# Kernel tuning notes

Measured on AMD Instinct MI355X. Metric: run time of the kernel, lower is better.

The kernel has to match this reference:

```python
import jax, jax.numpy as jnp
import numpy as np

EPS = 1e-5      # BatchNorm2d default eps
SLOPE = 0.01    # F.leaky_relu default negative slope


def _bn(h, gamma, beta):
    # training-mode BatchNorm2d with batch=1: normalize per channel over the
    # N x N spatial extent (channels are the last axis here).
    mean = jnp.mean(h, axis=(0, 1))
    var = jnp.var(h, axis=(0, 1))  # biased variance, as torch uses for normalization
    return (h - mean) * jax.lax.rsqrt(var + EPS) * gamma + beta


def _block(h, W, b, gamma, beta):
    # 1x1 conv == per-position channel matmul; layout [N, N, C]
    h = jnp.einsum('nmc,oc->nmo', h, W) + b
    return jax.nn.leaky_relu(_bn(h, gamma, beta), SLOPE)


def setup_inputs() -> dict:
    key = jax.random.key(0)
    ks = jax.random.split(key, 12)
    N, C = 1536, 64
    H = [16, 16, 8, 8]  # nf * ratio
    x = jax.random.normal(ks[0], (N, C), dtype=jnp.float32)
    def w(k, o, i):
        return jax.random.normal(k, (o, i), dtype=jnp.float32) * (1.0 / np.sqrt(i))
    inp = {
        'x': x,
        'W1': w(ks[1], H[0], C),   'b1': jnp.zeros((H[0],), jnp.float32),
        'g1': jnp.ones((H[0],), jnp.float32), 'be1': jnp.zeros((H[0],), jnp.float32),
        'W2': w(ks[2], H[1], H[0]), 'b2': jnp.zeros((H[1],), jnp.float32),
        'g2': jnp.ones((H[1],), jnp.float32), 'be2': jnp.zeros((H[1],), jnp.float32),
        'W3': w(ks[3], H[2], H[1]), 'b3': jnp.zeros((H[2],), jnp.float32),
        'g3': jnp.ones((H[2],), jnp.float32), 'be3': jnp.zeros((H[2],), jnp.float32),
        'W4': w(ks[4], H[3], H[2]), 'b4': jnp.zeros((H[3],), jnp.float32),
        'g4': jnp.ones((H[3],), jnp.float32), 'be4': jnp.zeros((H[3],), jnp.float32),
        'W5': w(ks[5], 1, H[3]),    'b5': jnp.zeros((1,), jnp.float32),
    }
    return inp


def reference(x, W1, b1, g1, be1, W2, b2, g2, be2, W3, b3, g3, be3,
              W4, b4, g4, be4, W5, b5):
    # pairwise abs-diff adjacency features: [N, N, C]
    adj = jnp.abs(x[:, None, :] - x[None, :, :])
    h = _block(adj, W1, b1, g1, be1)
    h = _block(h, W2, b2, g2, be2)
    h = _block(h, W3, b3, g3, be3)
    h = _block(h, W4, b4, g4, be4)
    out = jnp.einsum('nmc,oc->nmo', h, W5) + b5  # [N, N, 1]
    return out[..., 0]  # [N, N]
```

## Files before the change

kernel.cpp:

```cpp
#include <hip/hip_runtime.h>
#include <stdint.h>


#define NPTS 1536
#define NTILES 4656
static constexpr float FNN   = 2359296.0f;
static constexpr float EPS   = 1e-5f;
static constexpr float SLOPE = 0.01f;
static constexpr float INV_M = 1.0f / 2359296.0f;

typedef __attribute__((ext_vector_type(8)))  short bf16x8;
typedef __attribute__((ext_vector_type(4)))  float f32x4;
typedef __attribute__((ext_vector_type(16))) float f32x16;
union frag8 { int4 i; bf16x8 v; };

__device__ __forceinline__ float bflo(unsigned u) {
    return __builtin_bit_cast(float, u << 16);
}
__device__ __forceinline__ float bfhi(unsigned u) {
    return __builtin_bit_cast(float, u & 0xffff0000u);
}
__device__ __forceinline__ unsigned short f2bf(float f) {
    unsigned u = __builtin_bit_cast(unsigned, f);
    u += 0x7fffu + ((u >> 16) & 1u);
    return (unsigned short)(u >> 16);
}
__device__ __forceinline__ unsigned pack2(float lo, float hi) {
    return (unsigned)f2bf(lo) | ((unsigned)f2bf(hi) << 16);
}
__device__ __forceinline__ unsigned packtr(float lo, float hi) {
    unsigned a = __builtin_bit_cast(unsigned, lo);
    unsigned b = __builtin_bit_cast(unsigned, hi);
#if __has_builtin(__builtin_amdgcn_perm)
    return __builtin_amdgcn_perm(b, a, 0x07060302u);
#else
    return (a >> 16) | (b & 0xffff0000u);
#endif
}
__device__ __forceinline__ float lrelu(float t) {
    return fmaxf(t, t * SLOPE);
}
__device__ __forceinline__ float4 ld4(const float* p) {
    return *(const float4*)p;
}
__device__ __forceinline__ unsigned shflx32(unsigned v) {
    return (unsigned)__shfl_xor((int)v, 32);
}

__device__ __forceinline__ int2 tri_decode(int t) {
    float disc = 37249.0f - 8.0f * (float)t;
    int mt = (int)((193.0f - sqrtf(disc)) * 0.5f);
    if (mt < 0) mt = 0;
    if (mt > 95) mt = 95;
    while (96 * (mt + 1) - ((mt + 1) * mt) / 2 <= t) mt++;
    while (96 * mt - (mt * (mt - 1)) / 2 > t) mt--;
    int nc = mt + (t - (96 * mt - (mt * (mt - 1)) / 2));
    return make_int2(mt, nc);
}

__device__ __forceinline__ void bn8_inline(
        const float* __restrict__ stats, const float* __restrict__ g,
        const float* __restrict__ be, float* sc, float* sh) {
#pragma unroll
    for (int c = 0; c < 8; c++) {
        float S = stats[c] + stats[16 + c] + stats[32 + c] + stats[48 + c];
        float Q = stats[8 + c] + stats[24 + c] + stats[40 + c] +
                  stats[56 + c];
        float mu  = S * INV_M;
        float var = fmaf(-mu, mu, Q * INV_M);
        float s   = g[c] * rsqrtf(var + EPS);
        sc[c] = s;
        sh[c] = fmaf(-mu, s, be[c]);
    }
}

__global__ __launch_bounds__(256) void k_prep(float* __restrict__ ws) {
    int t = blockIdx.x * 256 + threadIdx.x;
    if (t < 384) ws[t] = 0.0f;
}

__global__ __launch_bounds__(256) void k_layer1(
        const float* __restrict__ x, const float* __restrict__ W1,
        const float* __restrict__ b1, unsigned short* __restrict__ outb,
        float* __restrict__ stats) {
    int tid  = threadIdx.x;
    int lane = tid & 63;
    int wv   = tid >> 6;
    int gid  = blockIdx.x * 4 + wv;
    int2 tc  = tri_decode(gid);
    int mt   = tc.x;
    int nc   = tc.y;
    float wf = (mt == nc) ? 1.0f : 2.0f;
    int l15  = lane & 15;
    int quad = lane >> 4;
    int cb   = quad * 8;

    const float* wr = W1 + l15 * 64 + cb;
    float4 w0 = ld4(wr);
    float4 w1 = ld4(wr + 4);
    float4 w2 = ld4(wr + 32);
    float4 w3 = ld4(wr + 36);
    frag8 fb1, fb2;
    fb1.i = make_int4(pack2(w0.x, w0.y), pack2(w0.z, w0.w),
                      pack2(w1.x, w1.y), pack2(w1.z, w1.w));
    fb2.i = make_int4(pack2(w2.x, w2.y), pack2(w2.z, w2.w),
                      pack2(w3.x, w3.y), pack2(w3.z, w3.w));

    const float* xr = x + (mt * 16 + l15) * 64 + cb;
    float4 xa0 = ld4(xr);
    float4 xa1 = ld4(xr + 4);
    float4 xa2 = ld4(xr + 32);
    float4 xa3 = ld4(xr + 36);

    float4 b1v = ld4(b1 + quad * 4);
    float lsum[4] = {0.f, 0.f, 0.f, 0.f};
    float lssq[4] = {0.f, 0.f, 0.f, 0.f};

    int n0 = nc * 16;
    const float* xp = x + (size_t)n0 * 64 + cb;
    float4 uA0 = ld4(xp);
    float4 uA1 = ld4(xp + 4);
    float4 uA2 = ld4(xp + 32);
    float4 uA3 = ld4(xp + 36);
    const float* xq = x + (size_t)(n0 + 1) * 64 + cb;
    float4 uB0 = ld4(xq);
    float4 uB1 = ld4(xq + 4);
    float4 uB2 = ld4(xq + 32);
    float4 uB3 = ld4(xq + 36);

    auto body = [&](int i, float4& u0, float4& u1, float4& u2, float4& u3,
                    int pf) {
        frag8 fa1, fa2;
        fa1.i = make_int4(
            packtr(fabsf(xa0.x - u0.x), fabsf(xa0.y - u0.y)),
            packtr(fabsf(xa0.z - u0.z), fabsf(xa0.w - u0.w)),
            packtr(fabsf(xa1.x - u1.x), fabsf(xa1.y - u1.y)),
            packtr(fabsf(xa1.z - u1.z), fabsf(xa1.w - u1.w)));
        fa2.i = make_int4(
            packtr(fabsf(xa2.x - u2.x), fabsf(xa2.y - u2.y)),
            packtr(fabsf(xa2.z - u2.z), fabsf(xa2.w - u2.w)),
            packtr(fabsf(xa3.x - u3.x), fabsf(xa3.y - u3.y)),
            packtr(fabsf(xa3.z - u3.z), fabsf(xa3.w - u3.w)));
        const float* xf = x + (size_t)pf * 64 + cb;
        u0 = ld4(xf);
        u1 = ld4(xf + 4);
        u2 = ld4(xf + 32);
        u3 = ld4(xf + 36);
        f32x4 acc = {b1v.x, b1v.y, b1v.z, b1v.w};
        acc = __builtin_amdgcn_mfma_f32_16x16x32_bf16(fb1.v, fa1.v, acc, 0, 0, 0);
        acc = __builtin_amdgcn_mfma_f32_16x16x32_bf16(fb2.v, fa2.v, acc, 0, 0, 0);
        size_t pos = (size_t)gid * 256 + (size_t)i * 16 + l15;
#pragma unroll
        for (int r = 0; r < 4; r++) {
            lsum[r] += acc[r];
            lssq[r] = fmaf(acc[r], acc[r], lssq[r]);
        }
        *(uint2*)(outb + pos * 16 + quad * 4) =
            make_uint2(pack2(acc[0], acc[1]), pack2(acc[2], acc[3]));
    };

#pragma unroll 1
    for (int i = 0; i < 16; i += 2) {
        int pfA = n0 + ((i + 2 < 16) ? i + 2 : 15);
        int pfB = n0 + ((i + 3 < 16) ? i + 3 : 15);
        body(i,     uA0, uA1, uA2, uA3, pfA);
        body(i + 1, uB0, uB1, uB2, uB3, pfB);
    }

#pragma unroll
    for (int off = 1; off < 16; off <<= 1) {
#pragma unroll
        for (int r = 0; r < 4; r++) {
            lsum[r] += __shfl_xor(lsum[r], off);
            lssq[r] += __shfl_xor(lssq[r], off);
        }
    }
    __shared__ float red[4][32];
    if (l15 == 0) {
#pragma unroll
        for (int r = 0; r < 4; r++) {
            red[wv][quad * 4 + r]      = lsum[r] * wf;
            red[wv][16 + quad * 4 + r] = lssq[r] * wf;
        }
    }
    __syncthreads();
    if (tid < 32) {
        float v = red[0][tid] + red[1][tid] + red[2][tid] + red[3][tid];
        atomicAdd(stats + (blockIdx.x & 3) * 32 + tid, v);
    }
}

__global__ __launch_bounds__(256) void k_stats2(
        const unsigned short* __restrict__ h1,
        const float* __restrict__ stats1, const float* __restrict__ g1,
        const float* __restrict__ be1, const float* __restrict__ W2,
        float* __restrict__ raw2) {
    int tid  = threadIdx.x;
    int lane = tid & 63;
    int wv   = tid >> 6;
    int pc   = lane & 31;
    int kh   = lane >> 5;
    int gid  = blockIdx.x * 4 + wv;
    int2 tc  = tri_decode(gid);
    float wf = (tc.x == tc.y) ? 1.0f : 2.0f;

    float sc[8], sh[8];
#pragma unroll
    for (int j = 0; j < 8; j++) {
        int c = kh * 8 + j;
        float S = stats1[c] + stats1[32 + c] + stats1[64 + c] + stats1[96 + c];
        float Q = stats1[16 + c] + stats1[48 + c] + stats1[80 + c] +
                  stats1[112 + c];
        float mu  = S * INV_M;
        float var = fmaf(-mu, mu, Q * INV_M);
        float s   = g1[c] * rsqrtf(var + EPS);
        sc[j] = s;
        sh[j] = fmaf(-mu, s, be1[c]);
    }
    frag8 fw2; fw2.i = make_int4(0, 0, 0, 0);
    if (pc < 16) {
        const float* w = W2 + pc * 16 + kh * 8;
        float4 wa = ld4(w), wb = ld4(w + 4);
        fw2.i = make_int4(pack2(wa.x, wa.y), pack2(wa.z, wa.w),
                          pack2(wb.x, wb.y), pack2(wb.z, wb.w));
    }
    f32x16 z;
#pragma unroll
    for (int r = 0; r < 16; r++) z[r] = 0.0f;

    float sum[8], ssq[8];
#pragma unroll
    for (int r = 0; r < 8; r++) { sum[r] = 0.f; ssq[r] = 0.f; }

    size_t tile0 = (size_t)gid * 8;
    const unsigned short* ptr = h1 + (tile0 * 32 + pc) * 16 + kh * 8;

    auto proc = [&](uint4 v) {
        float a0 = bflo(v.x), a1 = bfhi(v.x);
        float a2 = bflo(v.y), a3 = bfhi(v.y);
        float a4 = bflo(v.z), a5 = bfhi(v.z);
        float a6 = bflo(v.w), a7 = bfhi(v.w);
        a0 = lrelu(fmaf(a0, sc[0], sh[0]));
        a1 = lrelu(fmaf(a1, sc[1], sh[1]));
        a2 = lrelu(fmaf(a2, sc[2], sh[2]));
        a3 = lrelu(fmaf(a3, sc[3], sh[3]));
        a4 = lrelu(fmaf(a4, sc[4], sh[4]));
        a5 = lrelu(fmaf(a5, sc[5], sh[5]));
        a6 = lrelu(fmaf(a6, sc[6], sh[6]));
        a7 = lrelu(fmaf(a7, sc[7], sh[7]));
        frag8 fb;
        fb.i = make_int4(packtr(a0, a1), packtr(a2, a3),
                         packtr(a4, a5), packtr(a6, a7));
        f32x16 d = __builtin_amdgcn_mfma_f32_32x32x16_bf16(fw2.v, fb.v, z, 0, 0, 0);
#pragma unroll
        for (int r = 0; r < 8; r++) {
            sum[r] += d[r];
            ssq[r] = fmaf(d[r], d[r], ssq[r]);
        }
    };

    uint4 vA = *(const uint4*)(ptr);
    uint4 vB = *(const uint4*)(ptr + 512);
#pragma unroll 1
    for (int p = 0; p < 4; p++) {
        uint4 nA = vA, nB = vB;
        if (p < 3) {
            nA = *(const uint4*)(ptr + (size_t)(2 * p + 2) * 512);
            nB = *(const uint4*)(ptr + (size_t)(2 * p + 3) * 512);
        }
        proc(vA);
        proc(vB);
        vA = nA; vB = nB;
    }

#pragma unroll
    for (int off = 1; off < 32; off <<= 1) {
#pragma unroll
        for (int r = 0; r < 8; r++) {
            sum[r] += __shfl_xor(sum[r], off);
            ssq[r] += __shfl_xor(ssq[r], off);
        }
    }
    __shared__ float red[4][32];
    if (pc == 0) {
#pragma unroll
        for (int r = 0; r < 8; r++) {
            int o = (r & 3) + 8 * (r >> 2) + 4 * kh;
            red[wv][o]      = sum[r] * wf;
            red[wv][16 + o] = ssq[r] * wf;
        }
    }
    __syncthreads();
    if (tid < 32) {
        float v = red[0][tid] + red[1][tid] + red[2][tid] + red[3][tid];
        atomicAdd(raw2 + (blockIdx.x & 3) * 32 + tid, v);
    }
}

__global__ __launch_bounds__(256) void k_fuse3(
        const unsigned short* __restrict__ h1,
        unsigned short* __restrict__ h3out,
        const float* __restrict__ stats1, const float* __restrict__ g1,
        const float* __restrict__ be1, const float* __restrict__ W2,
        const float* __restrict__ raw2, const float* __restrict__ g2,
        const float* __restrict__ be2, const float* __restrict__ b2,
        const float* __restrict__ W3, const float* __restrict__ b3,
        float* __restrict__ stats3) {
    int tid  = threadIdx.x;
    int lane = tid & 63;
    int wv   = tid >> 6;
    int pc   = lane & 31;
    int kh   = lane >> 5;
    int gid  = blockIdx.x * 4 + wv;
    int2 tc  = tri_decode(gid);
    float wf = (tc.x == tc.y) ? 1.0f : 2.0f;

    float sc[8], sh[8];
#pragma unroll
    for (int j = 0; j < 8; j++) {
        int c = kh * 8 + j;
        float S = stats1[c] + stats1[32 + c] + stats1[64 + c] + stats1[96 + c];
        float Q = stats1[16 + c] + stats1[48 + c] + stats1[80 + c] +
                  stats1[112 + c];
        float mu  = S * INV_M;
        float var = fmaf(-mu, mu, Q * INV_M);
        float s   = g1[c] * rsqrtf(var + EPS);
        sc[j] = s;
        sh[j] = fmaf(-mu, s, be1[c]);
    }
    float sc2[8], sh2[8];
#pragma unroll
    for (int r = 0; r < 8; r++) {
        int c = (r & 3) + 8 * (r >> 2) + 4 * kh;
        float S = raw2[c] + raw2[32 + c] + raw2[64 + c] + raw2[96 + c];
        float Q = raw2[16 + c] + raw2[48 + c] + raw2[80 + c] + raw2[112 + c];
        float bc = b2[c];
        float sm = S + FNN * bc;
        float sq = Q + 2.0f * bc * S + FNN * bc * bc;
        float mu  = sm * INV_M;
        float var = fmaf(-mu, mu, sq * INV_M);
        float s   = g2[c] * rsqrtf(var + EPS);
        float shv = fmaf(-mu, s, be2[c]);
        sc2[r] = s;
        sh2[r] = fmaf(s, bc, shv);
    }
    frag8 fw2; fw2.i = make_int4(0, 0, 0, 0);
    if (pc < 16) {
        const float* w = W2 + pc * 16 + kh * 8;
        float4 wa = ld4(w), wb = ld4(w + 4);
        fw2.i = make_int4(pack2(wa.x, wa.y), pack2(wa.z, wa.w),
                          pack2(wb.x, wb.y), pack2(wb.z, wb.w));
    }
    frag8 fw3; fw3.i = make_int4(0, 0, 0, 0);
    if (pc < 8) {
        const float* w = W3 + pc * 16 + kh * 8;
        float4 wa = ld4(w), wb = ld4(w + 4);
        fw3.i = make_int4(pack2(wa.x, wa.y), pack2(wa.z, wa.w),
                          pack2(wb.x, wb.y), pack2(wb.z, wb.w));
    }
    float b3r[4];
#pragma unroll
    for (int r = 0; r < 4; r++) b3r[r] = b3[kh * 4 + r];

    f32x16 z;
#pragma unroll
    for (int r = 0; r < 16; r++) z[r] = 0.0f;

    float sum3[4] = {0.f, 0.f, 0.f, 0.f}, ssq3[4] = {0.f, 0.f, 0.f, 0.f};

    size_t tile0 = (size_t)gid * 8;
    const unsigned short* ptr = h1 + (tile0 * 32 + pc) * 16 + kh * 8;

    uint4 v0 = *(const uint4*)(ptr);
    uint4 v1 = *(const uint4*)(ptr + 512);
#pragma unroll 1
    for (int it = 0; it < 8; it++) {
        uint4 nx = v0;
        if (it + 2 < 8)
            nx = *(const uint4*)(ptr + (size_t)(it + 2) * 512);
        float a0 = bflo(v0.x), a1 = bfhi(v0.x);
        float a2 = bflo(v0.y), a3 = bfhi(v0.y);
        float a4 = bflo(v0.z), a5 = bfhi(v0.z);
        float a6 = bflo(v0.w), a7 = bfhi(v0.w);
        a0 = lrelu(fmaf(a0, sc[0], sh[0]));
        a1 = lrelu(fmaf(a1, sc[1], sh[1]));
        a2 = lrelu(fmaf(a2, sc[2], sh[2]));
        a3 = lrelu(fmaf(a3, sc[3], sh[3]));
        a4 = lrelu(fmaf(a4, sc[4], sh[4]));
        a5 = lrelu(fmaf(a5, sc[5], sh[5]));
        a6 = lrelu(fmaf(a6, sc[6], sh[6]));
        a7 = lrelu(fmaf(a7, sc[7], sh[7]));
        frag8 fb;
        fb.i = make_int4(packtr(a0, a1), packtr(a2, a3),
                         packtr(a4, a5), packtr(a6, a7));
        f32x16 d = __builtin_amdgcn_mfma_f32_32x32x16_bf16(fw2.v, fb.v, z, 0, 0, 0);
        float t0 = lrelu(fmaf(d[0], sc2[0], sh2[0]));
        float t1 = lrelu(fmaf(d[1], sc2[1], sh2[1]));
        float t2 = lrelu(fmaf(d[2], sc2[2], sh2[2]));
        float t3 = lrelu(fmaf(d[3], sc2[3], sh2[3]));
        float t4 = lrelu(fmaf(d[4], sc2[4], sh2[4]));
        float t5 = lrelu(fmaf(d[5], sc2[5], sh2[5]));
        float t6 = lrelu(fmaf(d[6], sc2[6], sh2[6]));
        float t7 = lrelu(fmaf(d[7], sc2[7], sh2[7]));
        unsigned w0 = packtr(t0, t1), w1 = packtr(t2, t3);
        unsigned w2 = packtr(t4, t5), w3 = packtr(t6, t7);
        unsigned p0 = kh ? w0 : w2;
        unsigned p1 = kh ? w1 : w3;
        unsigned q0 = shflx32(p0);
        unsigned q1 = shflx32(p1);
        frag8 fb2;
        fb2.i = make_int4(kh ? q0 : w0, kh ? q1 : w1,
                          kh ? w2 : q0, kh ? w3 : q1);
        f32x16 d2 = __builtin_amdgcn_mfma_f32_32x32x16_bf16(fw3.v, fb2.v, z, 0, 0, 0);
        float h0 = d2[0] + b3r[0];
        float h1v = d2[1] + b3r[1];
        float h2 = d2[2] + b3r[2];
        float h3v = d2[3] + b3r[3];
        sum3[0] += h0;  ssq3[0] = fmaf(h0, h0, ssq3[0]);
        sum3[1] += h1v; ssq3[1] = fmaf(h1v, h1v, ssq3[1]);
        sum3[2] += h2;  ssq3[2] = fmaf(h2, h2, ssq3[2]);
        sum3[3] += h3v; ssq3[3] = fmaf(h3v, h3v, ssq3[3]);
        size_t pos = (tile0 + it) * 32 + pc;
        *(uint2*)(h3out + pos * 8 + kh * 4) =
            make_uint2(pack2(h0, h1v), pack2(h2, h3v));
        v0 = v1; v1 = nx;
    }
#pragma unroll
    for (int off = 1; off < 32; off <<= 1) {
#pragma unroll
        for (int r = 0; r < 4; r++) {
            sum3[r] += __shfl_xor(sum3[r], off);
            ssq3[r] += __shfl_xor(ssq3[r], off);
        }
    }
    __shared__ float red[4][16];
    if (pc == 0) {
#pragma unroll
        for (int r = 0; r < 4; r++) {
            red[wv][kh * 4 + r]     = sum3[r] * wf;
            red[wv][8 + kh * 4 + r] = ssq3[r] * wf;
        }
    }
    __syncthreads();
    if (tid < 16) {
        float v = red[0][tid] + red[1][tid] + red[2][tid] + red[3][tid];
        atomicAdd(stats3 + (blockIdx.x & 3) * 16 + tid, v);
    }
}

__global__ __launch_bounds__(256) void k_stats4(
        const unsigned short* __restrict__ h3,
        const float* __restrict__ stats3, const float* __restrict__ g3,
        const float* __restrict__ be3, const float* __restrict__ W4,
        const float* __restrict__ b4, float* __restrict__ stats4) {
    int tid = threadIdx.x;
    int og1 = tid & 1;

    float wtile[4];
#pragma unroll
    for (int p = 0; p < 4; p++) {
        int2 tc = tri_decode(blockIdx.x * 4 + p);
        wtile[p] = (tc.x == tc.y) ? 1.0f : 2.0f;
    }

    float sc[8], sh[8];
    bn8_inline(stats3, g3, be3, sc, sh);

    float w[4][8];
#pragma unroll
    for (int j = 0; j < 4; j++) {
        const float* wr = W4 + (og1 * 4 + j) * 8;
        float4 v0 = ld4(wr);
        float4 v1 = ld4(wr + 4);
        w[j][0] = v0.x; w[j][1] = v0.y; w[j][2] = v0.z; w[j][3] = v0.w;
        w[j][4] = v1.x; w[j][5] = v1.y; w[j][6] = v1.z; w[j][7] = v1.w;
    }
    float bi[4];
#pragma unroll
    for (int j = 0; j < 4; j++) bi[j] = b4[og1 * 4 + j];

    float sum[4] = {0.f, 0.f, 0.f, 0.f}, ssq[4] = {0.f, 0.f, 0.f, 0.f};

    size_t p0 = (size_t)blockIdx.x * 1024 + (tid >> 1);
    const uint4* src = (const uint4*)h3 + p0;

    auto proc = [&](uint4 v, float wf) {
        float a[8];
        a[0] = bflo(v.x); a[1] = bfhi(v.x); a[2] = bflo(v.y); a[3] = bfhi(v.y);
        a[4] = bflo(v.z); a[5] = bfhi(v.z); a[6] = bflo(v.w); a[7] = bfhi(v.w);
#pragma unroll
        for (int c = 0; c < 8; c++)
            a[c] = lrelu(fmaf(a[c], sc[c], sh[c]));
        float d[4] = {bi[0], bi[1], bi[2], bi[3]};
#pragma unroll
        for (int c = 0; c < 8; c++) {
#pragma unroll
            for (int j = 0; j < 4; j++)
                d[j] = fmaf(a[c], w[j][c], d[j]);
        }
#pragma unroll
        for (int j = 0; j < 4; j++) {
            float wd = wf * d[j];
            sum[j] += wd;
            ssq[j] = fmaf(wd, d[j], ssq[j]);
        }
    };

    uint4 vA = src[0];
    uint4 vB = src[128];
#pragma unroll 1
    for (int p = 0; p < 4; p++) {
        uint4 nA = vA, nB = vB;
        if (p < 3) {
            nA = src[(size_t)(2 * p + 2) * 128];
            nB = src[(size_t)(2 * p + 3) * 128];
        }
        proc(vA, wtile[p]);
        proc(vB, wtile[p]);
        vA = nA; vB = nB;
    }
#pragma unroll
    for (int off = 2; off < 64; off <<= 1) {
#pragma unroll
        for (int j = 0; j < 4; j++) {
            sum[j] += __shfl_xor(sum[j], off);
            ssq[j] += __shfl_xor(ssq[j], off);
        }
    }
    __shared__ float red[4][16];
    int wv = tid >> 6, lane = tid & 63;
    if (lane < 2) {
#pragma unroll
        for (int j = 0; j < 4; j++) {
            red[wv][og1 * 4 + j]     = sum[j];
            red[wv][8 + og1 * 4 + j] = ssq[j];
        }
    }
    __syncthreads();
    if (tid < 16) {
        float v = red[0][tid] + red[1][tid] + red[2][tid] + red[3][tid];
        atomicAdd(stats4 + (blockIdx.x & 3) * 16 + tid, v);
    }
}

__global__ __launch_bounds__(256) void k_last(
        const unsigned short* __restrict__ h3,
        const float* __restrict__ stats3, const float* __restrict__ g3,
        const float* __restrict__ be3, const float* __restrict__ stats4,
        const float* __restrict__ g4, const float* __restrict__ be4,
        const float* __restrict__ W4, const float* __restrict__ b4,
        const float* __restrict__ W5, const float* __restrict__ b5,
        float* __restrict__ out) {
    int tid = threadIdx.x;

    size_t p0 = (size_t)blockIdx.x * 1024 + tid;
    const uint4* src = (const uint4*)h3 + p0;
    uint4 vv[4];
    vv[0] = src[0];
    vv[1] = src[256];
    vv[2] = src[512];
    vv[3] = src[768];

    float sc3[8], sh3[8];
    bn8_inline(stats3, g3, be3, sc3, sh3);

    float w4f[8][8], b4f[8], w5[8];
#pragma unroll
    for (int o = 0; o < 8; o++) {
        float S = stats4[o] + stats4[16 + o] + stats4[32 + o] + stats4[48 + o];
        float Q = stats4[8 + o] + stats4[24 + o] + stats4[40 + o] +
                  stats4[56 + o];
        float mu  = S * INV_M;
        float var = fmaf(-mu, mu, Q * INV_M);
        float s   = g4[o] * rsqrtf(var + EPS);
        float shv = fmaf(-mu, s, be4[o]);
        b4f[o] = fmaf(s, b4[o], shv);
        const float* wr = W4 + o * 8;
        float4 v0 = ld4(wr);
        float4 v1 = ld4(wr + 4);
        w4f[o][0] = s * v0.x; w4f[o][1] = s * v0.y;
        w4f[o][2] = s * v0.z; w4f[o][3] = s * v0.w;
        w4f[o][4] = s * v1.x; w4f[o][5] = s * v1.y;
        w4f[o][6] = s * v1.z; w4f[o][7] = s * v1.w;
        w5[o] = W5[o];
    }
    float b5v = b5[0];

    int nl = tid >> 4, ml = tid & 15;
    int2 tcs[4];
#pragma unroll
    for (int it = 0; it < 4; it++)
        tcs[it] = tri_decode(blockIdx.x * 4 + it);

    __shared__ float T[4][272];

#pragma unroll
    for (int it = 0; it < 4; it++) {
        uint4 va = vv[it];
        float a[8];
        a[0] = bflo(va.x); a[1] = bfhi(va.x); a[2] = bflo(va.y); a[3] = bfhi(va.y);
        a[4] = bflo(va.z); a[5] = bfhi(va.z); a[6] = bflo(va.w); a[7] = bfhi(va.w);
#pragma unroll
        for (int c = 0; c < 8; c++)
            a[c] = lrelu(fmaf(a[c], sc3[c], sh3[c]));
        float acc = b5v;
#pragma unroll
        for (int o = 0; o < 8; o++) {
            float h = b4f[o];
#pragma unroll
            for (int c = 0; c < 8; c++)
                h = fmaf(a[c], w4f[o][c], h);
            acc = fmaf(lrelu(h), w5[o], acc);
        }
        int gn = tcs[it].y * 16 + nl;
        int gm = tcs[it].x * 16 + ml;
        out[(size_t)gn * NPTS + gm] = acc;
        T[it][nl * 17 + ml] = acc;
    }
    __syncthreads();
#pragma unroll
    for (int it = 0; it < 4; it++) {
        float mv = T[it][ml * 17 + nl];
        out[(size_t)(tcs[it].x * 16 + nl) * NPTS + tcs[it].y * 16 + ml] = mv;
    }
}

extern "C" void kernel_launch(void* const* d_in, const int* in_sizes, int n_in,
                              void* d_out, int out_size, void* d_ws,
                              size_t ws_size, hipStream_t stream) {
    const float* x   = (const float*)d_in[0];
    const float* W1  = (const float*)d_in[1];
    const float* b1  = (const float*)d_in[2];
    const float* g1  = (const float*)d_in[3];
    const float* be1 = (const float*)d_in[4];
    const float* W2  = (const float*)d_in[5];
    const float* b2  = (const float*)d_in[6];
    const float* g2  = (const float*)d_in[7];
    const float* be2 = (const float*)d_in[8];
    const float* W3  = (const float*)d_in[9];
    const float* b3  = (const float*)d_in[10];
    const float* g3  = (const float*)d_in[11];
    const float* be3 = (const float*)d_in[12];
    const float* W4  = (const float*)d_in[13];
    const float* b4  = (const float*)d_in[14];
    const float* g4  = (const float*)d_in[15];
    const float* be4 = (const float*)d_in[16];
    const float* W5  = (const float*)d_in[17];
    const float* b5  = (const float*)d_in[18];

    float* ws     = (float*)d_ws;
    float* stats1 = ws + 0;
    float* raw2   = ws + 128;
    float* stats3 = ws + 256;
    float* stats4 = ws + 320;
    unsigned short* bufA = (unsigned short*)((char*)d_ws + 8192);
    unsigned short* bufB =
        (unsigned short*)((char*)d_ws + 8192 + (size_t)NTILES * 256 * 32);

    k_prep<<<2, 256, 0, stream>>>(ws);
    k_layer1<<<1164, 256, 0, stream>>>(x, W1, b1, bufA, stats1);
    k_stats2<<<1164, 256, 0, stream>>>(bufA, stats1, g1, be1, W2, raw2);
    k_fuse3<<<1164, 256, 0, stream>>>(bufA, bufB, stats1, g1, be1, W2,
                                      raw2, g2, be2, b2, W3, b3, stats3);
    k_stats4<<<1164, 256, 0, stream>>>(bufB, stats3, g3, be3, W4, b4, stats4);
    k_last<<<1164, 256, 0, stream>>>(bufB, stats3, g3, be3, stats4, g4, be4,
                                     W4, b4, W5, b5, (float*)d_out);
}
```

Before: 188.2 us.

## Fuse all layers into one cooperative kernel keeping activations in LDS

Replaces the five-kernel pipeline with a single cooperative kernel of 256 blocks. Each block owns up to 19 triangle tiles and keeps their layer-1 activations in shared memory, using grid-wide syncs between the BatchNorm statistics passes. This removes the global-memory round trips for the intermediate bf16 buffers and several kernel launches. The cost is very large LDS use (about 152KB per block), one block per CU with only 8 waves, and serialized grid barriers that may hurt latency hiding.

```diff
diff --git a/kernel.cpp b/kernel.cpp
--- a/kernel.cpp
+++ b/kernel.cpp
@@ -1,9 +1,14 @@
 #include <hip/hip_runtime.h>
+#include <hip/hip_cooperative_groups.h>
 #include <stdint.h>
+
+namespace cg = cooperative_groups;
 
 
 #define NPTS 1536
 #define NTILES 4656
+#define NBLK 256
+#define NTMAX 19
 static constexpr float FNN   = 2359296.0f;
 static constexpr float EPS   = 1e-5f;
 static constexpr float SLOPE = 0.01f;
@@ -79,549 +84,497 @@
     if (t < 384) ws[t] = 0.0f;
 }
 
-__global__ __launch_bounds__(256) void k_layer1(
-        const float* __restrict__ x, const float* __restrict__ W1,
-        const float* __restrict__ b1, unsigned short* __restrict__ outb,
-        float* __restrict__ stats) {
+__global__ __launch_bounds__(512, 2) void k_mega(
+        const float* __restrict__ x,
+        const float* __restrict__ W1, const float* __restrict__ b1,
+        const float* __restrict__ g1, const float* __restrict__ be1,
+        const float* __restrict__ W2, const float* __restrict__ b2,
+        const float* __restrict__ g2, const float* __restrict__ be2,
+        const float* __restrict__ W3, const float* __restrict__ b3,
+        const float* __restrict__ g3, const float* __restrict__ be3,
+        const float* __restrict__ W4, const float* __restrict__ b4,
+        const float* __restrict__ g4, const float* __restrict__ be4,
+        const float* __restrict__ W5, const float* __restrict__ b5,
+        float* __restrict__ out, float* __restrict__ ws) {
+
+    __shared__ unsigned short hbuf[NTMAX * 4096];
+    __shared__ float red[8][32];
+    __shared__ float Tm[2][272];
+    __shared__ int tdesc[NTMAX];
+
+    cg::grid_group grid = cg::this_grid();
+
     int tid  = threadIdx.x;
+    int bid  = blockIdx.x;
+    int w    = tid >> 6;
     int lane = tid & 63;
-    int wv   = tid >> 6;
-    int gid  = blockIdx.x * 4 + wv;
-    int2 tc  = tri_decode(gid);
-    int mt   = tc.x;
-    int nc   = tc.y;
-    float wf = (mt == nc) ? 1.0f : 2.0f;
-    int l15  = lane & 15;
-    int quad = lane >> 4;
-    int cb   = quad * 8;
-
-    const float* wr = W1 + l15 * 64 + cb;
-    float4 w0 = ld4(wr);
-    float4 w1 = ld4(wr + 4);
-    float4 w2 = ld4(wr + 32);
-    float4 w3 = ld4(wr + 36);
-    frag8 fb1, fb2;
-    fb1.i = make_int4(pack2(w0.x, w0.y), pack2(w0.z, w0.w),
-                      pack2(w1.x, w1.y), pack2(w1.z, w1.w));
-    fb2.i = make_int4(pack2(w2.x, w2.y), pack2(w2.z, w2.w),
-                      pack2(w3.x, w3.y), pack2(w3.z, w3.w));
-
-    const float* xr = x + (mt * 16 + l15) * 64 + cb;
-    float4 xa0 = ld4(xr);
-    float4 xa1 = ld4(xr + 4);
-    float4 xa2 = ld4(xr + 32);
-    float4 xa3 = ld4(xr + 36);
-
-    float4 b1v = ld4(b1 + quad * 4);
-    float lsum[4] = {0.f, 0.f, 0.f, 0.f};
-    float lssq[4] = {0.f, 0.f, 0.f, 0.f};
-
-    int n0 = nc * 16;
-    const float* xp = x + (size_t)n0 * 64 + cb;
-    float4 uA0 = ld4(xp);
-    float4 uA1 = ld4(xp + 4);
-    float4 uA2 = ld4(xp + 32);
-    float4 uA3 = ld4(xp + 36);
-    const float* xq = x + (size_t)(n0 + 1) * 64 + cb;
-    float4 uB0 = ld4(xq);
-    float4 uB1 = ld4(xq + 4);
-    float4 uB2 = ld4(xq + 32);
-    float4 uB3 = ld4(xq + 36);
-
-    auto body = [&](int i, float4& u0, float4& u1, float4& u2, float4& u3,
-                    int pf) {
-        frag8 fa1, fa2;
-        fa1.i = make_int4(
-            packtr(fabsf(xa0.x - u0.x), fabsf(xa0.y - u0.y)),
-            packtr(fabsf(xa0.z - u0.z), fabsf(xa0.w - u0.w)),
-            packtr(fabsf(xa1.x - u1.x), fabsf(xa1.y - u1.y)),
-            packtr(fabsf(xa1.z - u1.z), fabsf(xa1.w - u1.w)));
-        fa2.i = make_int4(
-            packtr(fabsf(xa2.x - u2.x), fabsf(xa2.y - u2.y)),
-            packtr(fabsf(xa2.z - u2.z), fabsf(xa2.w - u2.w)),
-            packtr(fabsf(xa3.x - u3.x), fabsf(xa3.y - u3.y)),
-            packtr(fabsf(xa3.z - u3.z), fabsf(xa3.w - u3.w)));
-        const float* xf = x + (size_t)pf * 64 + cb;
-        u0 = ld4(xf);
-        u1 = ld4(xf + 4);
-        u2 = ld4(xf + 32);
-        u3 = ld4(xf + 36);
-        f32x4 acc = {b1v.x, b1v.y, b1v.z, b1v.w};
-        acc = __builtin_amdgcn_mfma_f32_16x16x32_bf16(fb1.v, fa1.v, acc, 0, 0, 0);
-        acc = __builtin_amdgcn_mfma_f32_16x16x32_bf16(fb2.v, fa2.v, acc, 0, 0, 0);
-        size_t pos = (size_t)gid * 256 + (size_t)i * 16 + l15;
-#pragma unroll
-        for (int r = 0; r < 4; r++) {
-            lsum[r] += acc[r];
-            lssq[r] = fmaf(acc[r], acc[r], lssq[r]);
-        }
-        *(uint2*)(outb + pos * 16 + quad * 4) =
-            make_uint2(pack2(acc[0], acc[1]), pack2(acc[2], acc[3]));
-    };
-
-#pragma unroll 1
-    for (int i = 0; i < 16; i += 2) {
-        int pfA = n0 + ((i + 2 < 16) ? i + 2 : 15);
-        int pfB = n0 + ((i + 3 < 16) ? i + 3 : 15);
-        body(i,     uA0, uA1, uA2, uA3, pfA);
-        body(i + 1, uB0, uB1, uB2, uB3, pfB);
-    }
-
-#pragma unroll
-    for (int off = 1; off < 16; off <<= 1) {
-#pragma unroll
-        for (int r = 0; r < 4; r++) {
-            lsum[r] += __shfl_xor(lsum[r], off);
-            lssq[r] += __shfl_xor(lssq[r], off);
-        }
-    }
-    __shared__ float red[4][32];
-    if (l15 == 0) {
-#pragma unroll
-        for (int r = 0; r < 4; r++) {
-            red[wv][quad * 4 + r]      = lsum[r] * wf;
-            red[wv][16 + quad * 4 + r] = lssq[r] * wf;
-        }
+    int NT   = 18 + (bid < 48 ? 1 : 0);
+
+    float* stats1 = ws;
+    float* raw2   = ws + 128;
+    float* stats3 = ws + 256;
+    float* stats4 = ws + 320;
+    int rep32 = (bid & 3) * 32;
+    int rep16 = (bid & 3) * 16;
+
+    if (tid < NT) {
+        int2 tc = tri_decode(bid + NBLK * tid);
+        tdesc[tid] = (tc.x << 8) | tc.y;
     }
     __syncthreads();
-    if (tid < 32) {
-        float v = red[0][tid] + red[1][tid] + red[2][tid] + red[3][tid];
-        atomicAdd(stats + (blockIdx.x & 3) * 32 + tid, v);
+
+    {
+        int l15 = lane & 15, quad = lane >> 4, cb = quad * 8;
+        const float* wr = W1 + l15 * 64 + cb;
+        float4 w0 = ld4(wr);
+        float4 w1v = ld4(wr + 4);
+        float4 w2v = ld4(wr + 32);
+        float4 w3v = ld4(wr + 36);
+        frag8 fb1, fb2;
+        fb1.i = make_int4(pack2(w0.x, w0.y), pack2(w0.z, w0.w),
+                          pack2(w1v.x, w1v.y), pack2(w1v.z, w1v.w));
+        fb2.i = make_int4(pack2(w2v.x, w2v.y), pack2(w2v.z, w2v.w),
+                          pack2(w3v.x, w3v.y), pack2(w3v.z, w3v.w));
+        float4 b1v = ld4(b1 + quad * 4);
+        float lsum[4] = {0.f, 0.f, 0.f, 0.f};
+        float lssq[4] = {0.f, 0.f, 0.f, 0.f};
+
+#pragma unroll 1
+        for (int i = 0; i < NT; i++) {
+            int td = tdesc[i];
+            int mt = td >> 8, nc = td & 255;
+            float wf = (mt == nc) ? 1.0f : 2.0f;
+            const float* xr = x + (mt * 16 + l15) * 64 + cb;
+            float4 xa0 = ld4(xr);
+            float4 xa1 = ld4(xr + 4);
+            float4 xa2 = ld4(xr + 32);
+            float4 xa3 = ld4(xr + 36);
+            int n0 = nc * 16;
+#pragma unroll
+            for (int jj = 0; jj < 2; jj++) {
+                int j = 2 * w + jj;
+                const float* xp = x + (size_t)(n0 + j) * 64 + cb;
+                float4 u0 = ld4(xp);
+                float4 u1 = ld4(xp + 4);
+                float4 u2 = ld4(xp + 32);
+                float4 u3 = ld4(xp + 36);
+                frag8 fa1, fa2;
+                fa1.i = make_int4(
+                    packtr(fabsf(xa0.x - u0.x), fabsf(xa0.y - u0.y)),
+                    packtr(fabsf(xa0.z - u0.z), fabsf(xa0.w - u0.w)),
+                    packtr(fabsf(xa1.x - u1.x), fabsf(xa1.y - u1.y)),
+                    packtr(fabsf(xa1.z - u1.z), fabsf(xa1.w - u1.w)));
+                fa2.i = make_int4(
+                    packtr(fabsf(xa2.x - u2.x), fabsf(xa2.y - u2.y)),
+                    packtr(fabsf(xa2.z - u2.z), fabsf(xa2.w - u2.w)),
+                    packtr(fabsf(xa3.x - u3.x), fabsf(xa3.y - u3.y)),
+                    packtr(fabsf(xa3.z - u3.z), fabsf(xa3.w - u3.w)));
+                f32x4 acc = {b1v.x, b1v.y, b1v.z, b1v.w};
+                acc = __builtin_amdgcn_mfma_f32_16x16x32_bf16(fb1.v, fa1.v,
+                                                              acc, 0, 0, 0);
+                acc = __builtin_amdgcn_mfma_f32_16x16x32_bf16(fb2.v, fa2.v,
+                                                              acc, 0, 0, 0);
+#pragma unroll
+                for (int r = 0; r < 4; r++) {
+                    float wa = wf * acc[r];
+                    lsum[r] += wa;
+                    lssq[r] = fmaf(wa, acc[r], lssq[r]);
+                }
+                *(uint2*)(hbuf + i * 4096 + j * 256 + l15 * 16 + quad * 4) =
+                    make_uint2(pack2(acc[0], acc[1]), pack2(acc[2], acc[3]));
+            }
+        }
+#pragma unroll
+        for (int off = 1; off < 16; off <<= 1) {
+#pragma unroll
+            for (int r = 0; r < 4; r++) {
+                lsum[r] += __shfl_xor(lsum[r], off);
+                lssq[r] += __shfl_xor(lssq[r], off);
+            }
+        }
+        if (l15 == 0) {
+#pragma unroll
+            for (int r = 0; r < 4; r++) {
+                red[w][quad * 4 + r]      = lsum[r];
+                red[w][16 + quad * 4 + r] = lssq[r];
+            }
+        }
+        __syncthreads();
+        if (tid < 32) {
+            float v = 0.f;
+#pragma unroll
+            for (int k = 0; k < 8; k++) v += red[k][tid];
+            atomicAdd(stats1 + rep32 + tid, v);
+        }
     }
-}
-
-__global__ __launch_bounds__(256) void k_stats2(
-        const unsigned short* __restrict__ h1,
-        const float* __restrict__ stats1, const float* __restrict__ g1,
-        const float* __restrict__ be1, const float* __restrict__ W2,
-        float* __restrict__ raw2) {
-    int tid  = threadIdx.x;
-    int lane = tid & 63;
-    int wv   = tid >> 6;
-    int pc   = lane & 31;
-    int kh   = lane >> 5;
-    int gid  = blockIdx.x * 4 + wv;
-    int2 tc  = tri_decode(gid);
-    float wf = (tc.x == tc.y) ? 1.0f : 2.0f;
-
-    float sc[8], sh[8];
-#pragma unroll
-    for (int j = 0; j < 8; j++) {
-        int c = kh * 8 + j;
-        float S = stats1[c] + stats1[32 + c] + stats1[64 + c] + stats1[96 + c];
-        float Q = stats1[16 + c] + stats1[48 + c] + stats1[80 + c] +
-                  stats1[112 + c];
-        float mu  = S * INV_M;
-        float var = fmaf(-mu, mu, Q * INV_M);
-        float s   = g1[c] * rsqrtf(var + EPS);
-        sc[j] = s;
-        sh[j] = fmaf(-mu, s, be1[c]);
+    grid.sync();
+
+    {
+        int pc = lane & 31, kh = lane >> 5;
+        float sc[8], sh[8];
+#pragma unroll
+        for (int jc = 0; jc < 8; jc++) {
+            int c = kh * 8 + jc;
+            float S = stats1[c] + stats1[32 + c] + stats1[64 + c] +
+                      stats1[96 + c];
+            float Q = stats1[16 + c] + stats1[48 + c] + stats1[80 + c] +
+                      stats1[112 + c];
+            float mu  = S * INV_M;
+            float var = fmaf(-mu, mu, Q * INV_M);
+            float s   = g1[c] * rsqrtf(var + EPS);
+            sc[jc] = s;
+            sh[jc] = fmaf(-mu, s, be1[c]);
+        }
+        frag8 fw2; fw2.i = make_int4(0, 0, 0, 0);
+        if (pc < 16) {
+            const float* wp = W2 + pc * 16 + kh * 8;
+            float4 wa = ld4(wp), wb = ld4(wp + 4);
+            fw2.i = make_int4(pack2(wa.x, wa.y), pack2(wa.z, wa.w),
+                              pack2(wb.x, wb.y), pack2(wb.z, wb.w));
+        }
+        f32x16 z;
+#pragma unroll
+        for (int r = 0; r < 16; r++) z[r] = 0.0f;
+        float sum2[8], ssq2[8];
+#pragma unroll
+        for (int r = 0; r < 8; r++) { sum2[r] = 0.f; ssq2[r] = 0.f; }
+
+#pragma unroll 1
+        for (int i = 0; i < NT; i++) {
+            int td = tdesc[i];
+            float wf = ((td >> 8) == (td & 255)) ? 1.0f : 2.0f;
+            uint4 v = *(const uint4*)(hbuf + i * 4096 + w * 512 + pc * 16 +
+                                      kh * 8);
+            float a0 = bflo(v.x), a1 = bfhi(v.x);
+            float a2 = bflo(v.y), a3 = bfhi(v.y);
+            float a4 = bflo(v.z), a5 = bfhi(v.z);
+            float a6 = bflo(v.w), a7 = bfhi(v.w);
+            a0 = lrelu(fmaf(a0, sc[0], sh[0]));
+            a1 = lrelu(fmaf(a1, sc[1], sh[1]));
+            a2 = lrelu(fmaf(a2, sc[2], sh[2]));
+            a3 = lrelu(fmaf(a3, sc[3], sh[3]));
+            a4 = lrelu(fmaf(a4, sc[4], sh[4]));
+            a5 = lrelu(fmaf(a5, sc[5], sh[5]));
+            a6 = lrelu(fmaf(a6, sc[6], sh[6]));
+            a7 = lrelu(fmaf(a7, sc[7], sh[7]));
+            frag8 fbv;
+            fbv.i = make_int4(packtr(a0, a1), packtr(a2, a3),
+                              packtr(a4, a5), packtr(a6, a7));
+            f32x16 d = __builtin_amdgcn_mfma_f32_32x32x16_bf16(fw2.v, fbv.v,
+                                                               z, 0, 0, 0);
+#pragma unroll
+            for (int r = 0; r < 8; r++) {
+                float dv = d[r];
+                float wd = wf * dv;
+                sum2[r] += wd;
+                ssq2[r] = fmaf(wd, dv, ssq2[r]);
+            }
+        }
+#pragma unroll
+        for (int off = 1; off < 32; off <<= 1) {
+#pragma unroll
+            for (int r = 0; r < 8; r++) {
+                sum2[r] += __shfl_xor(sum2[r], off);
+                ssq2[r] += __shfl_xor(ssq2[r], off);
+            }
+        }
+        if (pc == 0) {
+#pragma unroll
+            for (int r = 0; r < 8; r++) {
+                int o = (r & 3) + 8 * (r >> 2) + 4 * kh;
+                red[w][o]      = sum2[r];
+                red[w][16 + o] = ssq2[r];
+            }
+        }
+        __syncthreads();
+        if (tid < 32) {
+            float v = 0.f;
+#pragma unroll
+            for (int k = 0; k < 8; k++) v += red[k][tid];
+            atomicAdd(raw2 + rep32 + tid, v);
+        }
     }
-    frag8 fw2; fw2.i = make_int4(0, 0, 0, 0);
-    if (pc < 16) {
-        const float* w = W2 + pc * 16 + kh * 8;
-        float4 wa = ld4(w), wb = ld4(w + 4);
-        fw2.i = make_int4(pack2(wa.x, wa.y), pack2(wa.z, wa.w),
-                          pack2(wb.x, wb.y), pack2(wb.z, wb.w));
+    grid.sync();
+
+    {
+        int pc = lane & 31, kh = lane >> 5;
+        float sc[8], sh[8];
+#pragma unroll
+        for (int jc = 0; jc < 8; jc++) {
+            int c = kh * 8 + jc;
+            float S = stats1[c] + stats1[32 + c] + stats1[64 + c] +
+                      stats1[96 + c];
+            float Q = stats1[16 + c] + stats1[48 + c] + stats1[80 + c] +
+                      stats1[112 + c];
+            float mu  = S * INV_M;
+            float var = fmaf(-mu, mu, Q * INV_M);
+            float s   = g1[c] * rsqrtf(var + EPS);
+            sc[jc] = s;
+            sh[jc] = fmaf(-mu, s, be1[c]);
+        }
+        float sc2[8], sh2[8];
+#pragma unroll
+        for (int r = 0; r < 8; r++) {
+            int c = (r & 3) + 8 * (r >> 2) + 4 * kh;
+            float S = raw2[c] + raw2[32 + c] + raw2[64 + c] + raw2[96 + c];
+            float Q = raw2[16 + c] + raw2[48 + c] + raw2[80 + c] +
+                      raw2[112 + c];
+            float bc = b2[c];
+            float sm = S + FNN * bc;
+            float sq = Q + 2.0f * bc * S + FNN * bc * bc;
+            float mu  = sm * INV_M;
+            float var = fmaf(-mu, mu, sq * INV_M);
+            float s   = g2[c] * rsqrtf(var + EPS);
+            float shv = fmaf(-mu, s, be2[c]);
+            sc2[r] = s;
+            sh2[r] = fmaf(s, bc, shv);
+        }
+        frag8 fw2; fw2.i = make_int4(0, 0, 0, 0);
+        if (pc < 16) {
+            const float* wp = W2 + pc * 16 + kh * 8;
+            float4 wa = ld4(wp), wb = ld4(wp + 4);
+            fw2.i = make_int4(pack2(wa.x, wa.y), pack2(wa.z, wa.w),
+                              pack2(wb.x, wb.y), pack2(wb.z, wb.w));
+        }
+        frag8 fw3; fw3.i = make_int4(0, 0, 0, 0);
+        if (pc < 8) {
+            const float* wp = W3 + pc * 16 + kh * 8;
+            float4 wa = ld4(wp), wb = ld4(wp + 4);
+            fw3.i = make_int4(pack2(wa.x, wa.y), pack2(wa.z, wa.w),
+                              pack2(wb.x, wb.y), pack2(wb.z, wb.w));
+        }
+        float b3r[4];
+#pragma unroll
+        for (int r = 0; r < 4; r++) b3r[r] = b3[kh * 4 + r];
+        f32x16 z;
+#pragma unroll
+        for (int r = 0; r < 16; r++) z[r] = 0.0f;
+        float sum3[4] = {0.f, 0.f, 0.f, 0.f};
+        float ssq3[4] = {0.f, 0.f, 0.f, 0.f};
+
+#pragma unroll 1
+        for (int i = 0; i < NT; i++) {
+            int td = tdesc[i];
+            float wf = ((td >> 8) == (td & 255)) ? 1.0f : 2.0f;
+            uint4 v = *(const uint4*)(hbuf + i * 4096 + w * 512 + pc * 16 +
+                                      kh * 8);
+            __syncthreads();
+            float a0 = bflo(v.x), a1 = bfhi(v.x);
+            float a2 = bflo(v.y), a3 = bfhi(v.y);
+            float a4 = bflo(v.z), a5 = bfhi(v.z);
+            float a6 = bflo(v.w), a7 = bfhi(v.w);
+            a0 = lrelu(fmaf(a0, sc[0], sh[0]));
+            a1 = lrelu(fmaf(a1, sc[1], sh[1]));
+            a2 = lrelu(fmaf(a2, sc[2], sh[2]));
+            a3 = lrelu(fmaf(a3, sc[3], sh[3]));
+            a4 = lrelu(fmaf(a4, sc[4], sh[4]));
+            a5 = lrelu(fmaf(a5, sc[5], sh[5]));
+            a6 = lrelu(fmaf(a6, sc[6], sh[6]));
+            a7 = lrelu(fmaf(a7, sc[7], sh[7]));
+            frag8 fbv;
+            fbv.i = make_int4(packtr(a0, a1), packtr(a2, a3),
+                              packtr(a4, a5), packtr(a6, a7));
+            f32x16 d = __builtin_amdgcn_mfma_f32_32x32x16_bf16(fw2.v, fbv.v,
+                                                               z, 0, 0, 0);
+            float t0 = lrelu(fmaf(d[0], sc2[0], sh2[0]));
+            float t1 = lrelu(fmaf(d[1], sc2[1], sh2[1]));
+            float t2 = lrelu(fmaf(d[2], sc2[2], sh2[2]));
+            float t3 = lrelu(fmaf(d[3], sc2[3], sh2[3]));
+            float t4 = lrelu(fmaf(d[4], sc2[4], sh2[4]));
+            float t5 = lrelu(fmaf(d[5], sc2[5], sh2[5]));
+            float t6 = lrelu(fmaf(d[6], sc2[6], sh2[6]));
+            float t7 = lrelu(fmaf(d[7], sc2[7], sh2[7]));
+            unsigned e0 = packtr(t0, t1), e1 = packtr(t2, t3);
+            unsigned e2 = packtr(t4, t5), e3 = packtr(t6, t7);
+            unsigned p0 = kh ? e0 : e2;
+            unsigned p1 = kh ? e1 : e3;
+            unsigned q0 = shflx32(p0);
+            unsigned q1 = shflx32(p1);
+            frag8 fb2;
+            fb2.i = make_int4(kh ? q0 : e0, kh ? q1 : e1,
+                              kh ? e2 : q0, kh ? e3 : q1);
+            f32x16 d2 = __builtin_amdgcn_mfma_f32_32x32x16_bf16(fw3.v, fb2.v,
+                                                                z, 0, 0, 0);
+            float h0  = d2[0] + b3r[0];
+            float h1v = d2[1] + b3r[1];
+            float h2v = d2[2] + b3r[2];
+            float h3v = d2[3] + b3r[3];
+            float wh;
+            wh = wf * h0;  sum3[0] += wh; ssq3[0] = fmaf(wh, h0,  ssq3[0]);
+            wh = wf * h1v; sum3[1] += wh; ssq3[1] = fmaf(wh, h1v, ssq3[1]);
+            wh = wf * h2v; sum3[2] += wh; ssq3[2] = fmaf(wh, h2v, ssq3[2]);
+            wh = wf * h3v; sum3[3] += wh; ssq3[3] = fmaf(wh, h3v, ssq3[3]);
+            *(uint2*)(hbuf + i * 4096 + 2048 + w * 256 + pc * 8 + kh * 4) =
+                make_uint2(pack2(h0, h1v), pack2(h2v, h3v));
+        }
+#pragma unroll
+        for (int off = 1; off < 32; off <<= 1) {
+#pragma unroll
+            for (int r = 0; r < 4; r++) {
+                sum3[r] += __shfl_xor(sum3[r], off);
+                ssq3[r] += __shfl_xor(ssq3[r], off);
+            }
+        }
+        if (pc == 0) {
+#pragma unroll
+            for (int r = 0; r < 4; r++) {
+                red[w][kh * 4 + r]     = sum3[r];
+                red[w][8 + kh * 4 + r] = ssq3[r];
+            }
+        }
+        __syncthreads();
+        if (tid < 16) {
+            float v = 0.f;
+#pragma unroll
+            for (int k = 0; k < 8; k++) v += red[k][tid];
+            atomicAdd(stats3 + rep16 + tid, v);
+        }
     }
-    f32x16 z;
-#pragma unroll
-    for (int r = 0; r < 16; r++) z[r] = 0.0f;
-
-    float sum[8], ssq[8];
-#pragma unroll
-    for (int r = 0; r < 8; r++) { sum[r] = 0.f; ssq[r] = 0.f; }
-
-    size_t tile0 = (size_t)gid * 8;
-    const unsigned short* ptr = h1 + (tile0 * 32 + pc) * 16 + kh * 8;
-
-    auto proc = [&](uint4 v) {
-        float a0 = bflo(v.x), a1 = bfhi(v.x);
-        float a2 = bflo(v.y), a3 = bfhi(v.y);
-        float a4 = bflo(v.z), a5 = bfhi(v.z);
-        float a6 = bflo(v.w), a7 = bfhi(v.w);
-        a0 = lrelu(fmaf(a0, sc[0], sh[0]));
-        a1 = lrelu(fmaf(a1, sc[1], sh[1]));
-        a2 = lrelu(fmaf(a2, sc[2], sh[2]));
-        a3 = lrelu(fmaf(a3, sc[3], sh[3]));
-        a4 = lrelu(fmaf(a4, sc[4], sh[4]));
-        a5 = lrelu(fmaf(a5, sc[5], sh[5]));
-        a6 = lrelu(fmaf(a6, sc[6], sh[6]));
-        a7 = lrelu(fmaf(a7, sc[7], sh[7]));
-        frag8 fb;
-        fb.i = make_int4(packtr(a0, a1), packtr(a2, a3),
-                         packtr(a4, a5), packtr(a6, a7));
-        f32x16 d = __builtin_amdgcn_mfma_f32_32x32x16_bf16(fw2.v, fb.v, z, 0, 0, 0);
-#pragma unroll
-        for (int r = 0; r < 8; r++) {
-            sum[r] += d[r];
-            ssq[r] = fmaf(d[r], d[r], ssq[r]);
-        }
-    };
-
-    uint4 vA = *(const uint4*)(ptr);
-    uint4 vB = *(const uint4*)(ptr + 512);
+    grid.sync();
+
+    {
+        float sc3[8], sh3[8];
+        bn8_inline(stats3, g3, be3, sc3, sh3);
+        int og = tid >> 8;
+        int p  = tid & 255;
+        float wv4[4][8], bi[4];
+#pragma unroll
+        for (int jv = 0; jv < 4; jv++) {
+            const float* wr = W4 + (og * 4 + jv) * 8;
+            float4 v0 = ld4(wr);
+            float4 v1 = ld4(wr + 4);
+            wv4[jv][0] = v0.x; wv4[jv][1] = v0.y;
+            wv4[jv][2] = v0.z; wv4[jv][3] = v0.w;
+            wv4[jv][4] = v1.x; wv4[jv][5] = v1.y;
+            wv4[jv][6] = v1.z; wv4[jv][7] = v1.w;
+            bi[jv] = b4[og * 4 + jv];
+        }
+        float sum4[4] = {0.f, 0.f, 0.f, 0.f};
+        float ssq4[4] = {0.f, 0.f, 0.f, 0.f};
+
 #pragma unroll 1
-    for (int p = 0; p < 4; p++) {
-        uint4 nA = vA, nB = vB;
-        if (p < 3) {
-            nA = *(const uint4*)(ptr + (size_t)(2 * p + 2) * 512);
-            nB = *(const uint4*)(ptr + (size_t)(2 * p + 3) * 512);
-        }
-        proc(vA);
-        proc(vB);
-        vA = nA; vB = nB;
+        for (int i = 0; i < NT; i++) {
+            int td = tdesc[i];
+            float wf = ((td >> 8) == (td & 255)) ? 1.0f : 2.0f;
+            uint4 v = *(const uint4*)(hbuf + i * 4096 + 2048 + p * 8);
+            float a[8];
+            a[0] = bflo(v.x); a[1] = bfhi(v.x);
+            a[2] = bflo(v.y); a[3] = bfhi(v.y);
+            a[4] = bflo(v.z); a[5] = bfhi(v.z);
+            a[6] = bflo(v.w); a[7] = bfhi(v.w);
+#pragma unroll
+            for (int c = 0; c < 8; c++)
+                a[c] = lrelu(fmaf(a[c], sc3[c], sh3[c]));
+            float d[4] = {bi[0], bi[1], bi[2], bi[3]};
+#pragma unroll
+            for (int c = 0; c < 8; c++) {
+#pragma unroll
+                for (int jv = 0; jv < 4; jv++)
+                    d[jv] = fmaf(a[c], wv4[jv][c], d[jv]);
+            }
+#pragma unroll
+            for (int jv = 0; jv < 4; jv++) {
+                float wd = wf * d[jv];
+                sum4[jv] += wd;
+                ssq4[jv] = fmaf(wd, d[jv], ssq4[jv]);
+            }
+        }
+#pragma unroll
+        for (int off = 1; off < 64; off <<= 1) {
+#pragma unroll
+            for (int jv = 0; jv < 4; jv++) {
+                sum4[jv] += __shfl_xor(sum4[jv], off);
+                ssq4[jv] += __shfl_xor(ssq4[jv], off);
+            }
+        }
+        if (lane == 0) {
+#pragma unroll
+            for (int jv = 0; jv < 4; jv++) {
+                red[w][jv]     = sum4[jv];
+                red[w][4 + jv] = ssq4[jv];
+            }
+        }
+        __syncthreads();
+        if (tid < 16) {
+            int part = tid >> 3;
+            int o    = tid & 7;
+            int og2  = o >> 2;
+            int jv   = o & 3;
+            float v = 0.f;
+#pragma unroll
+            for (int k = 0; k < 4; k++) v += red[og2 * 4 + k][part * 4 + jv];
+            atomicAdd(stats4 + rep16 + tid, v);
+        }
     }
-
-#pragma unroll
-    for (int off = 1; off < 32; off <<= 1) {
-#pragma unroll
-        for (int r = 0; r < 8; r++) {
-            sum[r] += __shfl_xor(sum[r], off);
-            ssq[r] += __shfl_xor(ssq[r], off);
-        }
-    }
-    __shared__ float red[4][32];
-    if (pc == 0) {
-#pragma unroll
-        for (int r = 0; r < 8; r++) {
-            int o = (r & 3) + 8 * (r >> 2) + 4 * kh;
-            red[wv][o]      = sum[r] * wf;
-            red[wv][16 + o] = ssq[r] * wf;
-        }
-    }
-    __syncthreads();
-    if (tid < 32) {
-        float v = red[0][tid] + red[1][tid] + red[2][tid] + red[3][tid];
-        atomicAdd(raw2 + (blockIdx.x & 3) * 32 + tid, v);
-    }
-}
-
-__global__ __launch_bounds__(256) void k_fuse3(
-        const unsigned short* __restrict__ h1,
-        unsigned short* __restrict__ h3out,
-        const float* __restrict__ stats1, const float* __restrict__ g1,
-        const float* __restrict__ be1, const float* __restrict__ W2,
-        const float* __restrict__ raw2, const float* __restrict__ g2,
-        const float* __restrict__ be2, const float* __restrict__ b2,
-        const float* __restrict__ W3, const float* __restrict__ b3,
-        float* __restrict__ stats3) {
-    int tid  = threadIdx.x;
-    int lane = tid & 63;
-    int wv   = tid >> 6;
-    int pc   = lane & 31;
-    int kh   = lane >> 5;
-    int gid  = blockIdx.x * 4 + wv;
-    int2 tc  = tri_decode(gid);
-    float wf = (tc.x == tc.y) ? 1.0f : 2.0f;
-
-    float sc[8], sh[8];
-#pragma unroll
-    for (int j = 0; j < 8; j++) {
-        int c = kh * 8 + j;
-        float S = stats1[c] + stats1[32 + c] + stats1[64 + c] + stats1[96 + c];
-        float Q = stats1[16 + c] + stats1[48 + c] + stats1[80 + c] +
-                  stats1[112 + c];
-        float mu  = S * INV_M;
-        float var = fmaf(-mu, mu, Q * INV_M);
-        float s   = g1[c] * rsqrtf(var + EPS);
-        sc[j] = s;
-        sh[j] = fmaf(-mu, s, be1[c]);
-    }
-    float sc2[8], sh2[8];
-#pragma unroll
-    for (int r = 0; r < 8; r++) {
-        int c = (r & 3) + 8 * (r >> 2) + 4 * kh;
-        float S = raw2[c] + raw2[32 + c] + raw2[64 + c] + raw2[96 + c];
-        float Q = raw2[16 + c] + raw2[48 + c] + raw2[80 + c] + raw2[112 + c];
-        float bc = b2[c];
-        float sm = S + FNN * bc;
-        float sq = Q + 2.0f * bc * S + FNN * bc * bc;
-        float mu  = sm * INV_M;
-        float var = fmaf(-mu, mu, sq * INV_M);
-        float s   = g2[c] * rsqrtf(var + EPS);
-        float shv = fmaf(-mu, s, be2[c]);
-        sc2[r] = s;
-        sh2[r] = fmaf(s, bc, shv);
-    }
-    frag8 fw2; fw2.i = make_int4(0, 0, 0, 0);
-    if (pc < 16) {
-        const float* w = W2 + pc * 16 + kh * 8;
-        float4 wa = ld4(w), wb = ld4(w + 4);
-        fw2.i = make_int4(pack2(wa.x, wa.y), pack2(wa.z, wa.w),
-                          pack2(wb.x, wb.y), pack2(wb.z, wb.w));
-    }
-    frag8 fw3; fw3.i = make_int4(0, 0, 0, 0);
-    if (pc < 8) {
-        const float* w = W3 + pc * 16 + kh * 8;
-        float4 wa = ld4(w), wb = ld4(w + 4);
-        fw3.i = make_int4(pack2(wa.x, wa.y), pack2(wa.z, wa.w),
-                          pack2(wb.x, wb.y), pack2(wb.z, wb.w));
-    }
-    float b3r[4];
-#pragma unroll
-    for (int r = 0; r < 4; r++) b3r[r] = b3[kh * 4 + r];
-
-    f32x16 z;
-#pragma unroll
-    for (int r = 0; r < 16; r++) z[r] = 0.0f;
-
-    float sum3[4] = {0.f, 0.f, 0.f, 0.f}, ssq3[4] = {0.f, 0.f, 0.f, 0.f};
-
-    size_t tile0 = (size_t)gid * 8;
-    const unsigned short* ptr = h1 + (tile0 * 32 + pc) * 16 + kh * 8;
-
-    uint4 v0 = *(const uint4*)(ptr);
-    uint4 v1 = *(const uint4*)(ptr + 512);
+    grid.sync();
+
+    {
+        float sc3[8], sh3[8];
+        bn8_inline(stats3, g3, be3, sc3, sh3);
+        float w4f[8][8], b4f[8], w5r[8];
+#pragma unroll
+        for (int o = 0; o < 8; o++) {
+            float S = stats4[o] + stats4[16 + o] + stats4[32 + o] +
+                      stats4[48 + o];
+            float Q = stats4[8 + o] + stats4[24 + o] + stats4[40 + o] +
+                      stats4[56 + o];
+            float mu  = S * INV_M;
+            float var = fmaf(-mu, mu, Q * INV_M);
+            float s   = g4[o] * rsqrtf(var + EPS);
+            float shv = fmaf(-mu, s, be4[o]);
+            b4f[o] = fmaf(s, b4[o], shv);
+            const float* wr = W4 + o * 8;
+            float4 v0 = ld4(wr);
+            float4 v1 = ld4(wr + 4);
+            w4f[o][0] = s * v0.x; w4f[o][1] = s * v0.y;
+            w4f[o][2] = s * v0.z; w4f[o][3] = s * v0.w;
+            w4f[o][4] = s * v1.x; w4f[o][5] = s * v1.y;
+            w4f[o][6] = s * v1.z; w4f[o][7] = s * v1.w;
+            w5r[o] = W5[o];
+        }
+        float b5v = b5[0];
+        int half = tid >> 8;
+        int lt   = tid & 255;
+        int nl = lt >> 4, ml = lt & 15;
+        int npair = (NT + 1) >> 1;
+
 #pragma unroll 1
-    for (int it = 0; it < 8; it++) {
-        uint4 nx = v0;
-        if (it + 2 < 8)
-            nx = *(const uint4*)(ptr + (size_t)(it + 2) * 512);
-        float a0 = bflo(v0.x), a1 = bfhi(v0.x);
-        float a2 = bflo(v0.y), a3 = bfhi(v0.y);
-        float a4 = bflo(v0.z), a5 = bfhi(v0.z);
-        float a6 = bflo(v0.w), a7 = bfhi(v0.w);
-        a0 = lrelu(fmaf(a0, sc[0], sh[0]));
-        a1 = lrelu(fmaf(a1, sc[1], sh[1]));
-        a2 = lrelu(fmaf(a2, sc[2], sh[2]));
-        a3 = lrelu(fmaf(a3, sc[3], sh[3]));
-        a4 = lrelu(fmaf(a4, sc[4], sh[4]));
-        a5 = lrelu(fmaf(a5, sc[5], sh[5]));
-        a6 = lrelu(fmaf(a6, sc[6], sh[6]));
-        a7 = lrelu(fmaf(a7, sc[7], sh[7]));
-        frag8 fb;
-        fb.i = make_int4(packtr(a0, a1), packtr(a2, a3),
-                         packtr(a4, a5), packtr(a6, a7));
-        f32x16 d = __builtin_amdgcn_mfma_f32_32x32x16_bf16(fw2.v, fb.v, z, 0, 0, 0);
-        float t0 = lrelu(fmaf(d[0], sc2[0], sh2[0]));
-        float t1 = lrelu(fmaf(d[1], sc2[1], sh2[1]));
-        float t2 = lrelu(fmaf(d[2], sc2[2], sh2[2]));
-        float t3 = lrelu(fmaf(d[3], sc2[3], sh2[3]));
-        float t4 = lrelu(fmaf(d[4], sc2[4], sh2[4]));
-        float t5 = lrelu(fmaf(d[5], sc2[5], sh2[5]));
-        float t6 = lrelu(fmaf(d[6], sc2[6], sh2[6]));
-        float t7 = lrelu(fmaf(d[7], sc2[7], sh2[7]));
-        unsigned w0 = packtr(t0, t1), w1 = packtr(t2, t3);
-        unsigned w2 = packtr(t4, t5), w3 = packtr(t6, t7);
-        unsigned p0 = kh ? w0 : w2;
-        unsigned p1 = kh ? w1 : w3;
-        unsigned q0 = shflx32(p0);
-        unsigned q1 = shflx32(p1);
-        frag8 fb2;
-        fb2.i = make_int4(kh ? q0 : w0, kh ? q1 : w1,
-                          kh ? w2 : q0, kh ? w3 : q1);
-        f32x16 d2 = __builtin_amdgcn_mfma_f32_32x32x16_bf16(fw3.v, fb2.v, z, 0, 0, 0);
-        float h0 = d2[0] + b3r[0];
-        float h1v = d2[1] + b3r[1];
-        float h2 = d2[2] + b3r[2];
-        float h3v = d2[3] + b3r[3];
-        sum3[0] += h0;  ssq3[0] = fmaf(h0, h0, ssq3[0]);
-        sum3[1] += h1v; ssq3[1] = fmaf(h1v, h1v, ssq3[1]);
-        sum3[2] += h2;  ssq3[2] = fmaf(h2, h2, ssq3[2]);
-        sum3[3] += h3v; ssq3[3] = fmaf(h3v, h3v, ssq3[3]);
-        size_t pos = (tile0 + it) * 32 + pc;
-        *(uint2*)(h3out + pos * 8 + kh * 4) =
-            make_uint2(pack2(h0, h1v), pack2(h2, h3v));
-        v0 = v1; v1 = nx;
-    }
-#pragma unroll
-    for (int off = 1; off < 32; off <<= 1) {
-#pragma unroll
-        for (int r = 0; r < 4; r++) {
-            sum3[r] += __shfl_xor(sum3[r], off);
-            ssq3[r] += __shfl_xor(ssq3[r], off);
-        }
-    }
-    __shared__ float red[4][16];
-    if (pc == 0) {
-#pragma unroll
-        for (int r = 0; r < 4; r++) {
-            red[wv][kh * 4 + r]     = sum3[r] * wf;
-            red[wv][8 + kh * 4 + r] = ssq3[r] * wf;
-        }
-    }
-    __syncthreads();
-    if (tid < 16) {
-        float v = red[0][tid] + red[1][tid] + red[2][tid] + red[3][tid];
-        atomicAdd(stats3 + (blockIdx.x & 3) * 16 + tid, v);
-    }
-}
-
-__global__ __launch_bounds__(256) void k_stats4(
-        const unsigned short* __restrict__ h3,
-        const float* __restrict__ stats3, const float* __restrict__ g3,
-        const float* __restrict__ be3, const float* __restrict__ W4,
-        const float* __restrict__ b4, float* __restrict__ stats4) {
-    int tid = threadIdx.x;
-    int og1 = tid & 1;
-
-    float wtile[4];
-#pragma unroll
-    for (int p = 0; p < 4; p++) {
-        int2 tc = tri_decode(blockIdx.x * 4 + p);
-        wtile[p] = (tc.x == tc.y) ? 1.0f : 2.0f;
-    }
-
-    float sc[8], sh[8];
-    bn8_inline(stats3, g3, be3, sc, sh);
-
-    float w[4][8];
-#pragma unroll
-    for (int j = 0; j < 4; j++) {
-        const float* wr = W4 + (og1 * 4 + j) * 8;
-        float4 v0 = ld4(wr);
-        float4 v1 = ld4(wr + 4);
-        w[j][0] = v0.x; w[j][1] = v0.y; w[j][2] = v0.z; w[j][3] = v0.w;
-        w[j][4] = v1.x; w[j][5] = v1.y; w[j][6] = v1.z; w[j][7] = v1.w;
-    }
-    float bi[4];
-#pragma unroll
-    for (int j = 0; j < 4; j++) bi[j] = b4[og1 * 4 + j];
-
-    float sum[4] = {0.f, 0.f, 0.f, 0.f}, ssq[4] = {0.f, 0.f, 0.f, 0.f};
-
-    size_t p0 = (size_t)blockIdx.x * 1024 + (tid >> 1);
-    const uint4* src = (const uint4*)h3 + p0;
-
-    auto proc = [&](uint4 v, float wf) {
-        float a[8];
-        a[0] = bflo(v.x); a[1] = bfhi(v.x); a[2] = bflo(v.y); a[3] = bfhi(v.y);
-        a[4] = bflo(v.z); a[5] = bfhi(v.z); a[6] = bflo(v.w); a[7] = bfhi(v.w);
-#pragma unroll
-        for (int c = 0; c < 8; c++)
-            a[c] = lrelu(fmaf(a[c], sc[c], sh[c]));
-        float d[4] = {bi[0], bi[1], bi[2], bi[3]};
-#pragma unroll
-        for (int c = 0; c < 8; c++) {
-#pragma unroll
-            for (int j = 0; j < 4; j++)
-                d[j] = fmaf(a[c], w[j][c], d[j]);
-        }
-#pragma unroll
-        for (int j = 0; j < 4; j++) {
-            float wd = wf * d[j];
-            sum[j] += wd;
-            ssq[j] = fmaf(wd, d[j], ssq[j]);
-        }
-    };
-
-    uint4 vA = src[0];
-    uint4 vB = src[128];
-#pragma unroll 1
-    for (int p = 0; p < 4; p++) {
-        uint4 nA = vA, nB = vB;
-        if (p < 3) {
-            nA = src[(size_t)(2 * p + 2) * 128];
-            nB = src[(size_t)(2 * p + 3) * 128];
-        }
-        proc(vA, wtile[p]);
-        proc(vB, wtile[p]);
-        vA = nA; vB = nB;
-    }
-#pragma unroll
-    for (int off = 2; off < 64; off <<= 1) {
-#pragma unroll
-        for (int j = 0; j < 4; j++) {
-            sum[j] += __shfl_xor(sum[j], off);
-            ssq[j] += __shfl_xor(ssq[j], off);
-        }
-    }
-    __shared__ float red[4][16];
-    int wv = tid >> 6, lane = tid & 63;
-    if (lane < 2) {
-#pragma unroll
-        for (int j = 0; j < 4; j++) {
-            red[wv][og1 * 4 + j]     = sum[j];
-            red[wv][8 + og1 * 4 + j] = ssq[j];
-        }
-    }
-    __syncthreads();
-    if (tid < 16) {
-        float v = red[0][tid] + red[1][tid] + red[2][tid] + red[3][tid];
-        atomicAdd(stats4 + (blockIdx.x & 3) * 16 + tid, v);
-    }
-}
-
-__global__ __launch_bounds__(256) void k_last(
-        const unsigned short* __restrict__ h3,
-        const float* __restrict__ stats3, const float* __restrict__ g3,
-        const float* __restrict__ be3, const float* __restrict__ stats4,
-        const float* __restrict__ g4, const float* __restrict__ be4,
-        const float* __restrict__ W4, const float* __restrict__ b4,
-        const float* __restrict__ W5, const float* __restrict__ b5,
-        float* __restrict__ out) {
-    int tid = threadIdx.x;
-
-    size_t p0 = (size_t)blockIdx.x * 1024 + tid;
-    const uint4* src = (const uint4*)h3 + p0;
-    uint4 vv[4];
-    vv[0] = src[0];
-    vv[1] = src[256];
-    vv[2] = src[512];
-    vv[3] = src[768];
-
-    float sc3[8], sh3[8];
-    bn8_inline(stats3, g3, be3, sc3, sh3);
-
-    float w4f[8][8], b4f[8], w5[8];
-#pragma unroll
-    for (int o = 0; o < 8; o++) {
-        float S = stats4[o] + stats4[16 + o] + stats4[32 + o] + stats4[48 + o];
-        float Q = stats4[8 + o] + stats4[24 + o] + stats4[40 + o] +
-                  stats4[56 + o];
-        float mu  = S * INV_M;
-        float var = fmaf(-mu, mu, Q * INV_M);
-        float s   = g4[o] * rsqrtf(var + EPS);
-        float shv = fmaf(-mu, s, be4[o]);
-        b4f[o] = fmaf(s, b4[o], shv);
-        const float* wr = W4 + o * 8;
-        float4 v0 = ld4(wr);
-        float4 v1 = ld4(wr + 4);
-        w4f[o][0] = s * v0.x; w4f[o][1] = s * v0.y;
-        w4f[o][2] = s * v0.z; w4f[o][3] = s * v0.w;
-        w4f[o][4] = s * v1.x; w4f[o][5] = s * v1.y;
-        w4f[o][6] = s * v1.z; w4f[o][7] = s * v1.w;
-        w5[o] = W5[o];
-    }
-    float b5v = b5[0];
-
-    int nl = tid >> 4, ml = tid & 15;
-    int2 tcs[4];
-#pragma unroll
-    for (int it = 0; it < 4; it++)
-        tcs[it] = tri_decode(blockIdx.x * 4 + it);
-
-    __shared__ float T[4][272];
-
-#pragma unroll
-    for (int it = 0; it < 4; it++) {
-        uint4 va = vv[it];
-        float a[8];
-        a[0] = bflo(va.x); a[1] = bfhi(va.x); a[2] = bflo(va.y); a[3] = bfhi(va.y);
-        a[4] = bflo(va.z); a[5] = bfhi(va.z); a[6] = bflo(va.w); a[7] = bfhi(va.w);
-#pragma unroll
-        for (int c = 0; c < 8; c++)
-            a[c] = lrelu(fmaf(a[c], sc3[c], sh3[c]));
-        float acc = b5v;
-#pragma unroll
-        for (int o = 0; o < 8; o++) {
-            float h = b4f[o];
-#pragma unroll
-            for (int c = 0; c < 8; c++)
-                h = fmaf(a[c], w4f[o][c], h);
-            acc = fmaf(lrelu(h), w5[o], acc);
-        }
-        int gn = tcs[it].y * 16 + nl;
-        int gm = tcs[it].x * 16 + ml;
-        out[(size_t)gn * NPTS + gm] = acc;
-        T[it][nl * 17 + ml] = acc;
-    }
-    __syncthreads();
-#pragma unroll
-    for (int it = 0; it < 4; it++) {
-        float mv = T[it][ml * 17 + nl];
-        out[(size_t)(tcs[it].x * 16 + nl) * NPTS + tcs[it].y * 16 + ml] = mv;
+        for (int jp = 0; jp < npair; jp++) {
+            int i = 2 * jp + half;
+            bool act = (i < NT);
+            float accv = 0.0f;
+            int mt = 0, nc = 0;
+            if (act) {
+                int td = tdesc[i];
+                mt = td >> 8; nc = td & 255;
+                uint4 v = *(const uint4*)(hbuf + i * 4096 + 2048 + lt * 8);
+                float a[8];
+                a[0] = bflo(v.x); a[1] = bfhi(v.x);
+                a[2] = bflo(v.y); a[3] = bfhi(v.y);
+                a[4] = bflo(v.z); a[5] = bfhi(v.z);
+                a[6] = bflo(v.w); a[7] = bfhi(v.w);
+#pragma unroll
+                for (int c = 0; c < 8; c++)
+                    a[c] = lrelu(fmaf(a[c], sc3[c], sh3[c]));
+                accv = b5v;
+#pragma unroll
+                for (int o = 0; o < 8; o++) {
+                    float h = b4f[o];
+#pragma unroll
+                    for (int c = 0; c < 8; c++)
+                        h = fmaf(a[c], w4f[o][c], h);
+                    accv = fmaf(lrelu(h), w5r[o], accv);
+                }
+                out[(size_t)(nc * 16 + nl) * NPTS + mt * 16 + ml] = accv;
+                Tm[half][nl * 17 + ml] = accv;
+            }
+            __syncthreads();
+            if (act) {
+                float mv = Tm[half][ml * 17 + nl];
+                out[(size_t)(mt * 16 + nl) * NPTS + nc * 16 + ml] = mv;
+            }
+            __syncthreads();
+        }
     }
 }
 
@@ -648,21 +601,19 @@
     const float* W5  = (const float*)d_in[17];
     const float* b5  = (const float*)d_in[18];
 
-    float* ws     = (float*)d_ws;
-    float* stats1 = ws + 0;
-    float* raw2   = ws + 128;
-    float* stats3 = ws + 256;
-    float* stats4 = ws + 320;
-    unsigned short* bufA = (unsigned short*)((char*)d_ws + 8192);
-    unsigned short* bufB =
-        (unsigned short*)((char*)d_ws + 8192 + (size_t)NTILES * 256 * 32);
+    float* ws   = (float*)d_ws;
+    float* outp = (float*)d_out;
 
     k_prep<<<2, 256, 0, stream>>>(ws);
-    k_layer1<<<1164, 256, 0, stream>>>(x, W1, b1, bufA, stats1);
-    k_stats2<<<1164, 256, 0, stream>>>(bufA, stats1, g1, be1, W2, raw2);
-    k_fuse3<<<1164, 256, 0, stream>>>(bufA, bufB, stats1, g1, be1, W2,
-                                      raw2, g2, be2, b2, W3, b3, stats3);
-    k_stats4<<<1164, 256, 0, stream>>>(bufB, stats3, g3, be3, W4, b4, stats4);
-    k_last<<<1164, 256, 0, stream>>>(bufB, stats3, g3, be3, stats4, g4, be4,
-                                     W4, b4, W5, b5, (float*)d_out);
-}
+
+    void* args[] = {
+        (void*)&x,
+        (void*)&W1, (void*)&b1, (void*)&g1, (void*)&be1,
+        (void*)&W2, (void*)&b2, (void*)&g2, (void*)&be2,
+        (void*)&W3, (void*)&b3, (void*)&g3, (void*)&be3,
+        (void*)&W4, (void*)&b4, (void*)&g4, (void*)&be4,
+        (void*)&W5, (void*)&b5,
+        (void*)&outp, (void*)&ws};
+    hipLaunchCooperativeKernel((const void*)k_mega, dim3(NBLK), dim3(512),
+                               args, 0, stream);
+}
```

Result: slower. 277.1 us (+47.2%).
